# Kernel optimization log

Hardware: AMD Instinct MI355X
Metric: run time of the kernel (lower is better)

The kernel has to match this reference:

```python
import jax, jax.numpy as jnp
from jax import lax
import numpy as np

DIM = 256
D_STATE = 16
D_CONV = 4
EXPAND = 2
D_INNER = EXPAND * DIM          # 512
DT_RANK = (DIM + 15) // 16      # 16
EPS = 1e-5


def setup_inputs() -> dict:
    key = jax.random.key(0)
    ks = jax.random.split(key, 8)
    B, H, W = 8, 32, 32
    dt_init = 0.01  # softplus(b_dt) ~= dt_init at init (mamba-style)
    return {
        "x": jax.random.normal(ks[0], (B, DIM, H, W), jnp.float32),
        "ln_gamma": jnp.ones((DIM,), jnp.float32),
        "ln_beta": jnp.zeros((DIM,), jnp.float32),
        "W_in": jax.random.normal(ks[1], (DIM, 2 * D_INNER), jnp.float32) * 0.02,
        "conv_w": jax.random.normal(ks[2], (D_INNER, D_CONV), jnp.float32) * 0.2,
        "conv_b": jnp.zeros((D_INNER,), jnp.float32),
        "W_xproj": jax.random.normal(ks[3], (D_INNER, DT_RANK + 2 * D_STATE), jnp.float32) * 0.02,
        "W_dt": jax.random.normal(ks[4], (DT_RANK, D_INNER), jnp.float32) * 0.05,
        "b_dt": jnp.full((D_INNER,), float(np.log(np.expm1(dt_init))), jnp.float32),
        "A_log": jnp.log(jnp.broadcast_to(
            jnp.arange(1, D_STATE + 1, dtype=jnp.float32), (D_INNER, D_STATE))),
        "D_skip": jnp.ones((D_INNER,), jnp.float32),
        "W_out": jax.random.normal(ks[5], (D_INNER, DIM), jnp.float32) * 0.02,
    }


def _mamba_layer(x, ln_gamma, ln_beta, W_in, conv_w, conv_b, W_xproj,
                 W_dt, b_dt, A_log, D_skip, W_out):
    B, C, H, W = x.shape
    L = H * W
    # (B,C,H,W) -> (B, L, C)
    xf = x.transpose(0, 2, 3, 1).reshape(B, L, C)
    # LayerNorm over channel dim
    mu = xf.mean(-1, keepdims=True)
    var = ((xf - mu) ** 2).mean(-1, keepdims=True)
    xn = (xf - mu) * lax.rsqrt(var + EPS) * ln_gamma + ln_beta
    # in_proj -> u (ssm branch) and z (gate branch)
    xz = xn @ W_in                              # [B, L, 2*D_INNER]
    u, z = xz[..., :D_INNER], xz[..., D_INNER:]
    # causal depthwise conv1d over L, then SiLU
    uc = u.transpose(0, 2, 1)                   # [B, D_INNER, L]
    uc = lax.conv_general_dilated(
        uc, conv_w[:, None, :], window_strides=(1,),
        padding=[(D_CONV - 1, 0)], feature_group_count=D_INNER)
    u2 = jax.nn.silu(uc + conv_b[None, :, None]).transpose(0, 2, 1)  # [B, L, D_INNER]
    # input-dependent dt, B, C
    dbc = u2 @ W_xproj                          # [B, L, DT_RANK + 2*D_STATE]
    dt = jax.nn.softplus(dbc[..., :DT_RANK] @ W_dt + b_dt)            # [B, L, D_INNER]
    Bm = dbc[..., DT_RANK:DT_RANK + D_STATE]    # [B, L, D_STATE]
    Cm = dbc[..., DT_RANK + D_STATE:]           # [B, L, D_STATE]
    A = -jnp.exp(A_log)                         # [D_INNER, D_STATE]

    def step(h, ins):
        dt_t, B_t, C_t, u_t = ins               # [B,Din], [B,S], [B,S], [B,Din]
        dA = jnp.exp(dt_t[:, :, None] * A)      # [B, Din, S]
        h = dA * h + dt_t[:, :, None] * B_t[:, None, :] * u_t[:, :, None]
        y = jnp.einsum('bds,bs->bd', h, C_t)
        return h, y

    h0 = jnp.zeros((B, D_INNER, D_STATE), xf.dtype)
    xs = (dt.transpose(1, 0, 2), Bm.transpose(1, 0, 2),
          Cm.transpose(1, 0, 2), u2.transpose(1, 0, 2))
    _, ys = lax.scan(step, h0, xs)              # ys: [L, B, D_INNER]
    y = ys.transpose(1, 0, 2) + u2 * D_skip     # skip connection D*u
    y = y * jax.nn.silu(z)                      # gate
    o = y @ W_out                               # [B, L, C]
    return o.reshape(B, H, W, C).transpose(0, 3, 1, 2) + x


def reference(x, ln_gamma, ln_beta, W_in, conv_w, conv_b, W_xproj,
              W_dt, b_dt, A_log, D_skip, W_out):
    return _mamba_layer(x, ln_gamma, ln_beta, W_in, conv_w, conv_b, W_xproj,
                        W_dt, b_dt, A_log, D_skip, W_out)
```

## Files before the change

### kernel.cpp

```cpp
#include <hip/hip_runtime.h>
#include <hip/hip_bf16.h>
#include <math.h>

#define DIMC   256
#define DI     512
#define DS     16
#define DTR    16
#define NX     48
#define BATCH  8
#define LSEQ   1024
#define MROWS  8192
#define CHUNK  64
#define NC     (LSEQ / CHUNK)

typedef __attribute__((ext_vector_type(8))) short short8;
typedef __attribute__((ext_vector_type(4))) float f32x4;

__device__ __forceinline__ unsigned short f2bf(float v) {
  __hip_bfloat16 h = __float2bfloat16(v);
  return *reinterpret_cast<unsigned short*>(&h);
}

__device__ __forceinline__ float dpp_sum16(float v) {
  float t;
  t = __int_as_float(__builtin_amdgcn_mov_dpp(__float_as_int(v), 0xB1,  0xF, 0xF, true)); v += t;
  t = __int_as_float(__builtin_amdgcn_mov_dpp(__float_as_int(v), 0x4E,  0xF, 0xF, true)); v += t;
  t = __int_as_float(__builtin_amdgcn_mov_dpp(__float_as_int(v), 0x141, 0xF, 0xF, true)); v += t;
  t = __int_as_float(__builtin_amdgcn_mov_dpp(__float_as_int(v), 0x140, 0xF, 0xF, true)); v += t;
  return v;
}

__global__ __launch_bounds__(256) void prep_all(const float* __restrict__ W_in,
                                                const float* __restrict__ W_out,
                                                const float* __restrict__ W_xproj,
                                                const float* __restrict__ W_dt,
                                                unsigned short* __restrict__ Wib,
                                                unsigned short* __restrict__ Wob,
                                                unsigned short* __restrict__ Wxpb,
                                                unsigned short* __restrict__ Wdtb) {
  __shared__ float t[32][33];
  const int blk = blockIdx.x, tid = threadIdx.x;
  if (blk < 384) {
    const float* W; unsigned short* Wt; int K, N, bx, by;
    if (blk < 256) { W = W_in;  Wt = Wib; K = DIMC; N = 1024; bx = blk & 31; by = blk >> 5; }
    else           { W = W_out; Wt = Wob; K = DI;   N = DIMC; bx = (blk - 256) & 7; by = (blk - 256) >> 3; }
    int n0 = bx * 32, k0 = by * 32;
    int tx = tid & 31, ty = tid >> 5;
    for (int i = ty; i < 32; i += 8) t[i][tx] = W[(size_t)(k0 + i) * N + n0 + tx];
    __syncthreads();
    for (int i = ty; i < 32; i += 8)
      Wt[(size_t)(n0 + i) * K + k0 + tx] = f2bf(t[tx][i]);
  } else if (blk < 512) {
    int idx = (blk - 384) * 256 + tid;
    int n = idx >> 9, k = idx & 511;
    Wxpb[idx] = (n < NX) ? f2bf(W_xproj[(size_t)k * NX + n]) : (unsigned short)0;
  } else {
    int idx = (blk - 512) * 256 + tid;
    int n = idx >> 5, k = idx & 31;
    Wdtb[idx] = (k < DTR) ? f2bf(W_dt[(size_t)k * DI + n]) : (unsigned short)0;
  }
}

__global__ __launch_bounds__(256) void ln_kernel(const float* __restrict__ x,
                                                 const float* __restrict__ gamma,
                                                 const float* __restrict__ beta,
                                                 unsigned short* __restrict__ xnb) {
  __shared__ float sx[DIMC][67];
  __shared__ float smean[64], srs[64];
  const int b = blockIdx.y, l0 = blockIdx.x * 64;
  const int tid = threadIdx.x;
  {
    const int cbase = tid >> 2;
    const int lp = (tid & 3) * 16;
#pragma unroll
    for (int cg = 0; cg < 4; ++cg) {
      const int c = cg * 64 + cbase;
      const float* p = x + ((size_t)b * DIMC + c) * LSEQ + l0 + lp;
#pragma unroll
      for (int q = 0; q < 4; ++q) {
        float4 v = *(const float4*)(p + q * 4);
        sx[c][lp + q * 4 + 0] = v.x;
        sx[c][lp + q * 4 + 1] = v.y;
        sx[c][lp + q * 4 + 2] = v.z;
        sx[c][lp + q * 4 + 3] = v.w;
      }
    }
  }
  __syncthreads();
  {
    const int lane = tid & 63, w = tid >> 6;
    const int l = (w << 4) + (lane & 15);
    const int quad = lane >> 4;
    float sum = 0.f, sq = 0.f;
#pragma unroll 8
    for (int cc = 0; cc < 64; ++cc) {
      float v = sx[quad * 64 + cc][l];
      sum += v; sq += v * v;
    }
    sum += __shfl_xor(sum, 16); sq += __shfl_xor(sq, 16);
    sum += __shfl_xor(sum, 32); sq += __shfl_xor(sq, 32);
    if (quad == 0) {
      float mean = sum * (1.f / 256.f);
      float var  = sq * (1.f / 256.f) - mean * mean;
      smean[l] = mean; srs[l] = rsqrtf(var + 1e-5f);
    }
  }
  __syncthreads();
  {
    const float gg = gamma[tid], bb = beta[tid];
    const size_t base = ((size_t)b * LSEQ + l0) * DIMC + tid;
#pragma unroll 4
    for (int ll = 0; ll < 64; ++ll) {
      float v = (sx[tid][ll] - smean[ll]) * srs[ll] * gg + bb;
      xnb[base + (size_t)ll * DIMC] = f2bf(v);
    }
  }
}

#define GTM 128
#define GTN 64
#define GBK 32
__global__ __launch_bounds__(256) void gemm_bf16(const unsigned short* __restrict__ A,
                                                 const unsigned short* __restrict__ Bt,
                                                 float* __restrict__ C,
                                                 int M, int N, int K, int mode,
                                                 const float* __restrict__ X) {
  __shared__ unsigned short As[GTM][GBK];
  __shared__ unsigned short Bs[GTN][GBK];
  const int tid = threadIdx.x;
  const int lane = tid & 63, wave = tid >> 6;
  const int wm = wave >> 1, wn = wave & 1;
  const int quad = lane >> 4, l16 = lane & 15;
  const int m0 = blockIdx.y * GTM, n0 = blockIdx.x * GTN;

  f32x4 acc[4][2];
#pragma unroll
  for (int i = 0; i < 4; ++i)
#pragma unroll
    for (int j = 0; j < 2; ++j) acc[i][j] = (f32x4){0.f, 0.f, 0.f, 0.f};

  for (int k0 = 0; k0 < K; k0 += GBK) {
#pragma unroll
    for (int q = 0; q < 2; ++q) {
      int id = q * 256 + tid;
      int row = id >> 2, c = id & 3;
      uint4 v = *(const uint4*)(A + (size_t)(m0 + row) * K + k0 + c * 8);
      *(uint4*)&As[row][c * 8] = v;
    }
    {
      int row = tid >> 2, c = tid & 3;
      uint4 v = *(const uint4*)(Bt + (size_t)(n0 + row) * K + k0 + c * 8);
      *(uint4*)&Bs[row][c * 8] = v;
    }
    __syncthreads();
    short8 af[4], bfrag[2];
#pragma unroll
    for (int i = 0; i < 4; ++i)
      af[i] = *(const short8*)&As[wm * 64 + i * 16 + l16][quad * 8];
#pragma unroll
    for (int j = 0; j < 2; ++j)
      bfrag[j] = *(const short8*)&Bs[wn * 32 + j * 16 + l16][quad * 8];
#pragma unroll
    for (int i = 0; i < 4; ++i)
#pragma unroll
      for (int j = 0; j < 2; ++j)
        acc[i][j] = __builtin_amdgcn_mfma_f32_16x16x32_bf16(af[i], bfrag[j], acc[i][j], 0, 0, 0);
    __syncthreads();
  }

  if (mode == 0) {
#pragma unroll
    for (int i = 0; i < 4; ++i) {
      int rowb = wm * 64 + i * 16 + quad * 4;
#pragma unroll
      for (int j = 0; j < 2; ++j) {
        int n = n0 + wn * 32 + j * 16 + l16;
#pragma unroll
        for (int r = 0; r < 4; ++r)
          C[(size_t)(m0 + rowb + r) * N + n] = acc[i][j][r];
      }
    }
  } else {
#pragma unroll
    for (int i = 0; i < 4; ++i) {
      int m = m0 + wm * 64 + i * 16 + quad * 4;
      int b = m >> 10, l = m & 1023;
#pragma unroll
      for (int j = 0; j < 2; ++j) {
        int n = n0 + wn * 32 + j * 16 + l16;
        size_t o = (size_t)b * (DIMC * LSEQ) + (size_t)n * LSEQ + l;
        f32x4 xv = *(const f32x4*)(X + o);
        f32x4 rv = acc[i][j] + xv;
        *(f32x4*)(C + o) = rv;
      }
    }
  }
}

__global__ __launch_bounds__(256) void conv_silu(const float* __restrict__ xz,
                                                 const float* __restrict__ conv_w,
                                                 const float* __restrict__ conv_b,
                                                 float* __restrict__ u2,
                                                 unsigned int* __restrict__ u2b) {
  int idx = (blockIdx.x * 256 + threadIdx.x) * 2;
  int c = idx & (DI - 1);
  int m = idx >> 9;
  int l = m & 1023;
  float2 acc = *(const float2*)(conv_b + c);
  float4 w0 = *(const float4*)(conv_w + c * 4);
  float4 w1 = *(const float4*)(conv_w + c * 4 + 4);
  const float wa[4] = {w0.x, w0.y, w0.z, w0.w};
  const float wb[4] = {w1.x, w1.y, w1.z, w1.w};
#pragma unroll
  for (int k = 0; k < 4; ++k) {
    int lj = l - 3 + k;
    if (lj >= 0) {
      float2 v = *(const float2*)(xz + (size_t)(m - 3 + k) * 1024 + c);
      acc.x = fmaf(v.x, wa[k], acc.x);
      acc.y = fmaf(v.y, wb[k], acc.y);
    }
  }
  float vx = acc.x / (1.f + __expf(-acc.x));
  float vy = acc.y / (1.f + __expf(-acc.y));
  *(float2*)(u2 + idx) = make_float2(vx, vy);
  u2b[idx >> 1] = (unsigned int)f2bf(vx) | ((unsigned int)f2bf(vy) << 16);
}

__global__ __launch_bounds__(256) void xproj_dt(const unsigned short* __restrict__ u2b,
                                                const unsigned short* __restrict__ Wxpb,
                                                const unsigned short* __restrict__ Wdtb,
                                                const float* __restrict__ b_dt,
                                                float* __restrict__ dbc64,
                                                float* __restrict__ dtv) {
  __shared__ unsigned short Bs[64][512 + 8];
  __shared__ unsigned short sdbc[32][40];
  const int m0 = blockIdx.x * 32;
  const int tid = threadIdx.x, lane = tid & 63, w = tid >> 6;
  const int quad = lane >> 4, l16 = lane & 15;
#pragma unroll
  for (int q = 0; q < 16; ++q) {
    int id = q * 256 + tid;
    int row = id >> 6, c8 = id & 63;
    *(uint4*)&Bs[row][c8 * 8] = *(const uint4*)(Wxpb + (size_t)row * 512 + c8 * 8);
  }
  __syncthreads();
  f32x4 acc[2];
  acc[0] = (f32x4){0.f, 0.f, 0.f, 0.f};
  acc[1] = (f32x4){0.f, 0.f, 0.f, 0.f};
#pragma unroll 4
  for (int k0 = 0; k0 < 512; k0 += 32) {
    short8 af0 = *(const short8*)(u2b + (size_t)(m0 + l16) * 512 + k0 + quad * 8);
    short8 af1 = *(const short8*)(u2b + (size_t)(m0 + 16 + l16) * 512 + k0 + quad * 8);
    short8 bf  = *(const short8*)&Bs[w * 16 + l16][k0 + quad * 8];
    acc[0] = __builtin_amdgcn_mfma_f32_16x16x32_bf16(af0, bf, acc[0], 0, 0, 0);
    acc[1] = __builtin_amdgcn_mfma_f32_16x16x32_bf16(af1, bf, acc[1], 0, 0, 0);
  }
#pragma unroll
  for (int i = 0; i < 2; ++i)
#pragma unroll
    for (int r = 0; r < 4; ++r)
      dbc64[(size_t)(m0 + i * 16 + quad * 4 + r) * 64 + w * 16 + l16] = acc[i][r];
  if (w < 2) {
#pragma unroll
    for (int i = 0; i < 2; ++i)
#pragma unroll
      for (int r = 0; r < 4; ++r)
        sdbc[i * 16 + quad * 4 + r][w * 16 + l16] = f2bf(acc[i][r]);
  }
  __syncthreads();
  short8 af0 = *(const short8*)&sdbc[l16][quad * 8];
  short8 af1 = *(const short8*)&sdbc[16 + l16][quad * 8];
#pragma unroll
  for (int jn = 0; jn < 8; ++jn) {
    const int n0 = w * 128 + jn * 16;
    short8 bf = *(const short8*)(Wdtb + (size_t)(n0 + l16) * 32 + quad * 8);
    f32x4 a0 = (f32x4){0.f, 0.f, 0.f, 0.f}, a1 = a0;
    a0 = __builtin_amdgcn_mfma_f32_16x16x32_bf16(af0, bf, a0, 0, 0, 0);
    a1 = __builtin_amdgcn_mfma_f32_16x16x32_bf16(af1, bf, a1, 0, 0, 0);
    const float bd = b_dt[n0 + l16];
#pragma unroll
    for (int r = 0; r < 4; ++r) {
      float v = a0[r] + bd;
      dtv[(size_t)(m0 + quad * 4 + r) * DI + n0 + l16] = (v > 20.f) ? v : log1pf(__expf(v));
      float v2 = a1[r] + bd;
      dtv[(size_t)(m0 + 16 + quad * 4 + r) * DI + n0 + l16] = (v2 > 20.f) ? v2 : log1pf(__expf(v2));
    }
  }
}

__global__ __launch_bounds__(256) void scan_pass1(const float* __restrict__ dtv,
                                                  const float* __restrict__ u2,
                                                  const float* __restrict__ dbc64,
                                                  const float* __restrict__ A_log,
                                                  float* __restrict__ hend,
                                                  float* __restrict__ Ssum) {
  const int bb = blockIdx.x, dblk = blockIdx.y, cc = blockIdx.z;
  const int tid = threadIdx.x;
  const int di = tid >> 4, s = tid & 15;
  const int d = dblk * 16 + di;
  const float Ads = -__expf(A_log[d * DS + s]);

  __shared__ float2 sdu[CHUNK][16];
  __shared__ float  sB[CHUNK][16];
  {
    const int t0 = cc * CHUNK;
#pragma unroll
    for (int q = 0; q < 4; ++q) {
      int lin = q * 256 + tid;
      int tt = lin >> 4, dd = lin & 15;
      size_t m = (size_t)bb * LSEQ + t0 + tt;
      sdu[tt][dd] = make_float2(dtv[m * DI + dblk * 16 + dd], u2[m * DI + dblk * 16 + dd]);
      sB[tt][dd]  = dbc64[m * 64 + DTR + dd];
    }
  }
  __syncthreads();
  float h = 0.f, dtsum = 0.f;
#pragma unroll 4
  for (int tt = 0; tt < CHUNK; ++tt) {
    float2 du = sdu[tt][di];
    float Bv  = sB[tt][s];
    h = fmaf(__expf(du.x * Ads), h, du.x * du.y * Bv);
    dtsum += du.x;
  }
  size_t ci = ((size_t)(bb * NC + cc) * DI + d);
  hend[ci * DS + s] = h;
  if (s == 0) Ssum[ci] = dtsum;
}

__global__ __launch_bounds__(256) void scan_pass2(const float* __restrict__ A_log,
                                                  const float* __restrict__ hend,
                                                  const float* __restrict__ Ssum,
                                                  float* __restrict__ hin) {
  const int bb = blockIdx.x, dblk = blockIdx.y;
  const int tid = threadIdx.x;
  const int di = tid >> 4, s = tid & 15;
  const int d = dblk * 16 + di;
  const float Ads = -__expf(A_log[d * DS + s]);
  float h = 0.f;
  for (int cc = 0; cc < NC; ++cc) {
    size_t ci = ((size_t)(bb * NC + cc) * DI + d);
    hin[ci * DS + s] = h;
    h = fmaf(__expf(Ads * Ssum[ci]), h, hend[ci * DS + s]);
  }
}

__global__ __launch_bounds__(256) void scan_pass3(const float* __restrict__ dtv,
                                                  const float* __restrict__ u2,
                                                  const float* __restrict__ dbc64,
                                                  const float* __restrict__ xz,
                                                  const float* __restrict__ A_log,
                                                  const float* __restrict__ D_skip,
                                                  const float* __restrict__ hin,
                                                  unsigned short* __restrict__ yb) {
  const int bb = blockIdx.x, dblk = blockIdx.y, cc = blockIdx.z;
  const int tid = threadIdx.x;
  const int di = tid >> 4, s = tid & 15;
  const int d = dblk * 16 + di;
  const float Ads = -__expf(A_log[d * DS + s]);

  __shared__ float2 sdu[CHUNK][16];
  __shared__ float2 sBC[CHUNK][16];
  __shared__ float  sz[CHUNK][16], sy[CHUNK][16];
  const int t0 = cc * CHUNK;
#pragma unroll
  for (int q = 0; q < 4; ++q) {
    int lin = q * 256 + tid;
    int tt = lin >> 4, dd = lin & 15;
    size_t m = (size_t)bb * LSEQ + t0 + tt;
    sdu[tt][dd] = make_float2(dtv[m * DI + dblk * 16 + dd], u2[m * DI + dblk * 16 + dd]);
    sBC[tt][dd] = make_float2(dbc64[m * 64 + DTR + dd], dbc64[m * 64 + DTR + DS + dd]);
    sz [tt][dd] = xz[m * 1024 + DI + dblk * 16 + dd];
  }
  __syncthreads();
  float h = hin[((size_t)(bb * NC + cc) * DI + d) * DS + s];
#pragma unroll 4
  for (int tt = 0; tt < CHUNK; ++tt) {
    float2 du = sdu[tt][di];
    float2 bc = sBC[tt][s];
    h = fmaf(__expf(du.x * Ads), h, du.x * du.y * bc.x);
    float v = dpp_sum16(h * bc.y);
    if (s == 0) sy[tt][di] = v;
  }
  __syncthreads();
#pragma unroll
  for (int q = 0; q < 4; ++q) {
    int lin = q * 256 + tid;
    int tt = lin >> 4, dd = lin & 15;
    size_t m = (size_t)bb * LSEQ + t0 + tt;
    float yv = sy[tt][dd] + sdu[tt][dd].y * D_skip[dblk * 16 + dd];
    float z = sz[tt][dd];
    yv *= z / (1.f + __expf(-z));
    yb[m * DI + dblk * 16 + dd] = f2bf(yv);
  }
}

extern "C" void kernel_launch(void* const* d_in, const int* in_sizes, int n_in,
                              void* d_out, int out_size, void* d_ws, size_t ws_size,
                              hipStream_t stream) {
  const float* x       = (const float*)d_in[0];
  const float* ln_g    = (const float*)d_in[1];
  const float* ln_b    = (const float*)d_in[2];
  const float* W_in    = (const float*)d_in[3];
  const float* conv_w  = (const float*)d_in[4];
  const float* conv_b  = (const float*)d_in[5];
  const float* W_xproj = (const float*)d_in[6];
  const float* W_dt    = (const float*)d_in[7];
  const float* b_dt    = (const float*)d_in[8];
  const float* A_log   = (const float*)d_in[9];
  const float* D_skip  = (const float*)d_in[10];
  const float* W_out   = (const float*)d_in[11];
  float* out = (float*)d_out;

  float* ws    = (float*)d_ws;
  float* xz    = ws;
  float* u2    = xz   + (size_t)MROWS * 1024;
  float* dbc64 = u2   + (size_t)MROWS * DI;
  float* dtv   = dbc64 + (size_t)MROWS * 64;
  float* hend  = dtv  + (size_t)MROWS * DI;
  float* hin   = hend + (size_t)BATCH * NC * DI * DS;
  float* Ssum  = hin  + (size_t)BATCH * NC * DI * DS;
  unsigned short* u2b  = (unsigned short*)(Ssum + (size_t)BATCH * NC * DI);
  unsigned short* yb   = u2b + (size_t)MROWS * DI;
  unsigned short* xnb  = yb;
  unsigned short* Wib  = yb  + (size_t)MROWS * DI;
  unsigned short* Wob  = Wib + (size_t)DIMC * 1024;
  unsigned short* Wxpb = Wob + (size_t)DI * DIMC;
  unsigned short* Wdtb = Wxpb + (size_t)64 * 512;

  prep_all<<<576, 256, 0, stream>>>(W_in, W_out, W_xproj, W_dt, Wib, Wob, Wxpb, Wdtb);

  ln_kernel<<<dim3(LSEQ / 64, BATCH), 256, 0, stream>>>(x, ln_g, ln_b, xnb);

  gemm_bf16<<<dim3(1024 / GTN, MROWS / GTM), 256, 0, stream>>>(
      xnb, Wib, xz, MROWS, 1024, DIMC, 0, nullptr);

  conv_silu<<<(MROWS * DI) / 512, 256, 0, stream>>>(xz, conv_w, conv_b, u2,
                                                    (unsigned int*)u2b);

  xproj_dt<<<MROWS / 32, 256, 0, stream>>>(u2b, Wxpb, Wdtb, b_dt, dbc64, dtv);

  dim3 gp13(BATCH, DI / 16, NC);
  dim3 gp2(BATCH, DI / 16);
  scan_pass1<<<gp13, 256, 0, stream>>>(dtv, u2, dbc64, A_log, hend, Ssum);
  scan_pass2<<<gp2, 256, 0, stream>>>(A_log, hend, Ssum, hin);
  scan_pass3<<<gp13, 256, 0, stream>>>(dtv, u2, dbc64, xz, A_log, D_skip, hin, yb);

  gemm_bf16<<<dim3(DIMC / GTN, MROWS / GTM), 256, 0, stream>>>(
      yb, Wob, out, MROWS, DIMC, DI, 1, x);
}
```

Baseline: 212.2 us.

## Give each scan thread four states and 64 channels per block

Scan passes 1 and 3 now map each thread to one channel and four of the sixteen states, so a block covers 64 channels instead of 16. The shared-memory staging of dt, u, B, C and z is dropped in favour of direct global loads, with float4 reads for B and C. The output reduction across states shrinks from a 16-lane to a 4-lane DPP sum, and the gating epilogue reads z and u straight from global memory. The grid for these passes shrinks by four, which lowers parallelism and adds per-step global loads in the serial loop, in exchange for less redundant per-thread work and fewer cross-lane operations.

```diff
diff --git a/kernel.cpp b/kernel.cpp
--- a/kernel.cpp
+++ b/kernel.cpp
@@ -21,12 +21,10 @@
   return *reinterpret_cast<unsigned short*>(&h);
 }
 
-__device__ __forceinline__ float dpp_sum16(float v) {
+__device__ __forceinline__ float dpp_sum4(float v) {
   float t;
-  t = __int_as_float(__builtin_amdgcn_mov_dpp(__float_as_int(v), 0xB1,  0xF, 0xF, true)); v += t;
-  t = __int_as_float(__builtin_amdgcn_mov_dpp(__float_as_int(v), 0x4E,  0xF, 0xF, true)); v += t;
-  t = __int_as_float(__builtin_amdgcn_mov_dpp(__float_as_int(v), 0x141, 0xF, 0xF, true)); v += t;
-  t = __int_as_float(__builtin_amdgcn_mov_dpp(__float_as_int(v), 0x140, 0xF, 0xF, true)); v += t;
+  t = __int_as_float(__builtin_amdgcn_mov_dpp(__float_as_int(v), 0xB1, 0xF, 0xF, true)); v += t;
+  t = __int_as_float(__builtin_amdgcn_mov_dpp(__float_as_int(v), 0x4E, 0xF, 0xF, true)); v += t;
   return v;
 }
 
@@ -296,35 +294,29 @@
                                                   float* __restrict__ Ssum) {
   const int bb = blockIdx.x, dblk = blockIdx.y, cc = blockIdx.z;
   const int tid = threadIdx.x;
-  const int di = tid >> 4, s = tid & 15;
-  const int d = dblk * 16 + di;
-  const float Ads = -__expf(A_log[d * DS + s]);
-
-  __shared__ float2 sdu[CHUNK][16];
-  __shared__ float  sB[CHUNK][16];
-  {
-    const int t0 = cc * CHUNK;
-#pragma unroll
-    for (int q = 0; q < 4; ++q) {
-      int lin = q * 256 + tid;
-      int tt = lin >> 4, dd = lin & 15;
-      size_t m = (size_t)bb * LSEQ + t0 + tt;
-      sdu[tt][dd] = make_float2(dtv[m * DI + dblk * 16 + dd], u2[m * DI + dblk * 16 + dd]);
-      sB[tt][dd]  = dbc64[m * 64 + DTR + dd];
-    }
-  }
-  __syncthreads();
-  float h = 0.f, dtsum = 0.f;
+  const int dl = tid >> 2, q = tid & 3;
+  const int d = dblk * 64 + dl;
+  float4 Av = *(const float4*)(A_log + d * DS + q * 4);
+  float Ads[4] = {-__expf(Av.x), -__expf(Av.y), -__expf(Av.z), -__expf(Av.w)};
+  float h[4] = {0.f, 0.f, 0.f, 0.f};
+  float dtsum = 0.f;
+  const size_t mbase = (size_t)bb * LSEQ + cc * CHUNK;
 #pragma unroll 4
   for (int tt = 0; tt < CHUNK; ++tt) {
-    float2 du = sdu[tt][di];
-    float Bv  = sB[tt][s];
-    h = fmaf(__expf(du.x * Ads), h, du.x * du.y * Bv);
-    dtsum += du.x;
+    size_t m = mbase + tt;
+    float dtt = dtv[m * DI + d];
+    float uu  = u2 [m * DI + d];
+    float4 Bv = *(const float4*)(dbc64 + m * 64 + DTR + q * 4);
+    float common = dtt * uu;
+    h[0] = fmaf(__expf(dtt * Ads[0]), h[0], common * Bv.x);
+    h[1] = fmaf(__expf(dtt * Ads[1]), h[1], common * Bv.y);
+    h[2] = fmaf(__expf(dtt * Ads[2]), h[2], common * Bv.z);
+    h[3] = fmaf(__expf(dtt * Ads[3]), h[3], common * Bv.w);
+    dtsum += dtt;
   }
   size_t ci = ((size_t)(bb * NC + cc) * DI + d);
-  hend[ci * DS + s] = h;
-  if (s == 0) Ssum[ci] = dtsum;
+  *(float4*)(hend + ci * DS + q * 4) = make_float4(h[0], h[1], h[2], h[3]);
+  if (q == 0) Ssum[ci] = dtsum;
 }
 
 __global__ __launch_bounds__(256) void scan_pass2(const float* __restrict__ A_log,
@@ -352,45 +344,46 @@
                                                   const float* __restrict__ D_skip,
                                                   const float* __restrict__ hin,
                                                   unsigned short* __restrict__ yb) {
+  __shared__ float sy[CHUNK][64];
   const int bb = blockIdx.x, dblk = blockIdx.y, cc = blockIdx.z;
   const int tid = threadIdx.x;
-  const int di = tid >> 4, s = tid & 15;
-  const int d = dblk * 16 + di;
-  const float Ads = -__expf(A_log[d * DS + s]);
-
-  __shared__ float2 sdu[CHUNK][16];
-  __shared__ float2 sBC[CHUNK][16];
-  __shared__ float  sz[CHUNK][16], sy[CHUNK][16];
-  const int t0 = cc * CHUNK;
-#pragma unroll
-  for (int q = 0; q < 4; ++q) {
-    int lin = q * 256 + tid;
-    int tt = lin >> 4, dd = lin & 15;
-    size_t m = (size_t)bb * LSEQ + t0 + tt;
-    sdu[tt][dd] = make_float2(dtv[m * DI + dblk * 16 + dd], u2[m * DI + dblk * 16 + dd]);
-    sBC[tt][dd] = make_float2(dbc64[m * 64 + DTR + dd], dbc64[m * 64 + DTR + DS + dd]);
-    sz [tt][dd] = xz[m * 1024 + DI + dblk * 16 + dd];
-  }
-  __syncthreads();
-  float h = hin[((size_t)(bb * NC + cc) * DI + d) * DS + s];
+  const int dl = tid >> 2, q = tid & 3;
+  const int d = dblk * 64 + dl;
+  float4 Av = *(const float4*)(A_log + d * DS + q * 4);
+  float Ads[4] = {-__expf(Av.x), -__expf(Av.y), -__expf(Av.z), -__expf(Av.w)};
+  const size_t ci = ((size_t)(bb * NC + cc) * DI + d);
+  float4 h4 = *(const float4*)(hin + ci * DS + q * 4);
+  float h[4] = {h4.x, h4.y, h4.z, h4.w};
+  const size_t mbase = (size_t)bb * LSEQ + cc * CHUNK;
 #pragma unroll 4
   for (int tt = 0; tt < CHUNK; ++tt) {
-    float2 du = sdu[tt][di];
-    float2 bc = sBC[tt][s];
-    h = fmaf(__expf(du.x * Ads), h, du.x * du.y * bc.x);
-    float v = dpp_sum16(h * bc.y);
-    if (s == 0) sy[tt][di] = v;
+    size_t m = mbase + tt;
+    float dtt = dtv[m * DI + d];
+    float uu  = u2 [m * DI + d];
+    float4 Bv = *(const float4*)(dbc64 + m * 64 + DTR + q * 4);
+    float4 Cv = *(const float4*)(dbc64 + m * 64 + DTR + DS + q * 4);
+    float common = dtt * uu;
+    float yp;
+    h[0] = fmaf(__expf(dtt * Ads[0]), h[0], common * Bv.x); yp  = h[0] * Cv.x;
+    h[1] = fmaf(__expf(dtt * Ads[1]), h[1], common * Bv.y); yp = fmaf(h[1], Cv.y, yp);
+    h[2] = fmaf(__expf(dtt * Ads[2]), h[2], common * Bv.z); yp = fmaf(h[2], Cv.z, yp);
+    h[3] = fmaf(__expf(dtt * Ads[3]), h[3], common * Bv.w); yp = fmaf(h[3], Cv.w, yp);
+    yp = dpp_sum4(yp);
+    if (q == 0) sy[tt][dl] = yp;
   }
   __syncthreads();
-#pragma unroll
-  for (int q = 0; q < 4; ++q) {
-    int lin = q * 256 + tid;
-    int tt = lin >> 4, dd = lin & 15;
-    size_t m = (size_t)bb * LSEQ + t0 + tt;
-    float yv = sy[tt][dd] + sdu[tt][dd].y * D_skip[dblk * 16 + dd];
-    float z = sz[tt][dd];
+  const int ed = tid & 63, tq = tid >> 6;
+  const int dg = dblk * 64 + ed;
+  const float dsk = D_skip[dg];
+#pragma unroll 4
+  for (int it = 0; it < 16; ++it) {
+    int tt = it * 4 + tq;
+    size_t m = mbase + tt;
+    float z  = xz[m * 1024 + DI + dg];
+    float uu = u2[m * DI + dg];
+    float yv = sy[tt][ed] + uu * dsk;
     yv *= z / (1.f + __expf(-z));
-    yb[m * DI + dblk * 16 + dd] = f2bf(yv);
+    yb[m * DI + dg] = f2bf(yv);
   }
 }
 
@@ -439,7 +432,7 @@
 
   xproj_dt<<<MROWS / 32, 256, 0, stream>>>(u2b, Wxpb, Wdtb, b_dt, dbc64, dtv);
 
-  dim3 gp13(BATCH, DI / 16, NC);
+  dim3 gp13(BATCH, DI / 64, NC);
   dim3 gp2(BATCH, DI / 16);
   scan_pass1<<<gp13, 256, 0, stream>>>(dtv, u2, dbc64, A_log, hend, Ssum);
   scan_pass2<<<gp2, 256, 0, stream>>>(A_log, hend, Ssum, hin);
```

Result: slower. 220.2 us (+3.8%).

## Merge weight prep with LayerNorm and fold inter-chunk scan into pass3

Applied to the files above, without the earlier changes.

Weight conversion and LayerNorm now run in one prologue kernel using extra block indices. The separate scan_pass2 kernel is removed. Each pass3 block recomputes its incoming chunk state by looping over all earlier chunk summaries, overlapped with its shared-memory loads. This cuts two kernel launches and the hin buffer round trip, at the cost of redundant serial work that grows with chunk index, up to 15 steps.

```diff
diff --git a/kernel.cpp b/kernel.cpp
--- a/kernel.cpp
+++ b/kernel.cpp
@@ -30,17 +30,23 @@
   return v;
 }
 
-__global__ __launch_bounds__(256) void prep_all(const float* __restrict__ W_in,
+__global__ __launch_bounds__(256) void prologue(const float* __restrict__ W_in,
                                                 const float* __restrict__ W_out,
                                                 const float* __restrict__ W_xproj,
                                                 const float* __restrict__ W_dt,
+                                                const float* __restrict__ x,
+                                                const float* __restrict__ gamma,
+                                                const float* __restrict__ beta,
                                                 unsigned short* __restrict__ Wib,
                                                 unsigned short* __restrict__ Wob,
                                                 unsigned short* __restrict__ Wxpb,
-                                                unsigned short* __restrict__ Wdtb) {
-  __shared__ float t[32][33];
+                                                unsigned short* __restrict__ Wdtb,
+                                                unsigned short* __restrict__ xnb) {
+  __shared__ float sx[DIMC][67];
+  __shared__ float smean[64], srs[64];
   const int blk = blockIdx.x, tid = threadIdx.x;
   if (blk < 384) {
+    float (*t)[67] = sx;
     const float* W; unsigned short* Wt; int K, N, bx, by;
     if (blk < 256) { W = W_in;  Wt = Wib; K = DIMC; N = 1024; bx = blk & 31; by = blk >> 5; }
     else           { W = W_out; Wt = Wob; K = DI;   N = DIMC; bx = (blk - 256) & 7; by = (blk - 256) >> 3; }
@@ -50,25 +56,22 @@
     __syncthreads();
     for (int i = ty; i < 32; i += 8)
       Wt[(size_t)(n0 + i) * K + k0 + tx] = f2bf(t[tx][i]);
-  } else if (blk < 512) {
+    return;
+  }
+  if (blk < 512) {
     int idx = (blk - 384) * 256 + tid;
     int n = idx >> 9, k = idx & 511;
     Wxpb[idx] = (n < NX) ? f2bf(W_xproj[(size_t)k * NX + n]) : (unsigned short)0;
-  } else {
+    return;
+  }
+  if (blk < 576) {
     int idx = (blk - 512) * 256 + tid;
     int n = idx >> 5, k = idx & 31;
     Wdtb[idx] = (k < DTR) ? f2bf(W_dt[(size_t)k * DI + n]) : (unsigned short)0;
-  }
-}
-
-__global__ __launch_bounds__(256) void ln_kernel(const float* __restrict__ x,
-                                                 const float* __restrict__ gamma,
-                                                 const float* __restrict__ beta,
-                                                 unsigned short* __restrict__ xnb) {
-  __shared__ float sx[DIMC][67];
-  __shared__ float smean[64], srs[64];
-  const int b = blockIdx.y, l0 = blockIdx.x * 64;
-  const int tid = threadIdx.x;
+    return;
+  }
+  const int lb = blk - 576;
+  const int b = lb >> 4, l0 = (lb & 15) * 64;
   {
     const int cbase = tid >> 2;
     const int lp = (tid & 3) * 16;
@@ -327,30 +330,14 @@
   if (s == 0) Ssum[ci] = dtsum;
 }
 
-__global__ __launch_bounds__(256) void scan_pass2(const float* __restrict__ A_log,
-                                                  const float* __restrict__ hend,
-                                                  const float* __restrict__ Ssum,
-                                                  float* __restrict__ hin) {
-  const int bb = blockIdx.x, dblk = blockIdx.y;
-  const int tid = threadIdx.x;
-  const int di = tid >> 4, s = tid & 15;
-  const int d = dblk * 16 + di;
-  const float Ads = -__expf(A_log[d * DS + s]);
-  float h = 0.f;
-  for (int cc = 0; cc < NC; ++cc) {
-    size_t ci = ((size_t)(bb * NC + cc) * DI + d);
-    hin[ci * DS + s] = h;
-    h = fmaf(__expf(Ads * Ssum[ci]), h, hend[ci * DS + s]);
-  }
-}
-
 __global__ __launch_bounds__(256) void scan_pass3(const float* __restrict__ dtv,
                                                   const float* __restrict__ u2,
                                                   const float* __restrict__ dbc64,
                                                   const float* __restrict__ xz,
                                                   const float* __restrict__ A_log,
                                                   const float* __restrict__ D_skip,
-                                                  const float* __restrict__ hin,
+                                                  const float* __restrict__ hend,
+                                                  const float* __restrict__ Ssum,
                                                   unsigned short* __restrict__ yb) {
   const int bb = blockIdx.x, dblk = blockIdx.y, cc = blockIdx.z;
   const int tid = threadIdx.x;
@@ -371,8 +358,12 @@
     sBC[tt][dd] = make_float2(dbc64[m * 64 + DTR + dd], dbc64[m * 64 + DTR + DS + dd]);
     sz [tt][dd] = xz[m * 1024 + DI + dblk * 16 + dd];
   }
-  __syncthreads();
-  float h = hin[((size_t)(bb * NC + cc) * DI + d) * DS + s];
+  float h = 0.f;
+  for (int j = 0; j < cc; ++j) {
+    size_t cj = ((size_t)(bb * NC + j) * DI + d);
+    h = fmaf(__expf(Ads * Ssum[cj]), h, hend[cj * DS + s]);
+  }
+  __syncthreads();
 #pragma unroll 4
   for (int tt = 0; tt < CHUNK; ++tt) {
     float2 du = sdu[tt][di];
@@ -417,8 +408,7 @@
   float* dbc64 = u2   + (size_t)MROWS * DI;
   float* dtv   = dbc64 + (size_t)MROWS * 64;
   float* hend  = dtv  + (size_t)MROWS * DI;
-  float* hin   = hend + (size_t)BATCH * NC * DI * DS;
-  float* Ssum  = hin  + (size_t)BATCH * NC * DI * DS;
+  float* Ssum  = hend + (size_t)BATCH * NC * DI * DS;
   unsigned short* u2b  = (unsigned short*)(Ssum + (size_t)BATCH * NC * DI);
   unsigned short* yb   = u2b + (size_t)MROWS * DI;
   unsigned short* xnb  = yb;
@@ -427,9 +417,8 @@
   unsigned short* Wxpb = Wob + (size_t)DI * DIMC;
   unsigned short* Wdtb = Wxpb + (size_t)64 * 512;
 
-  prep_all<<<576, 256, 0, stream>>>(W_in, W_out, W_xproj, W_dt, Wib, Wob, Wxpb, Wdtb);
-
-  ln_kernel<<<dim3(LSEQ / 64, BATCH), 256, 0, stream>>>(x, ln_g, ln_b, xnb);
+  prologue<<<704, 256, 0, stream>>>(W_in, W_out, W_xproj, W_dt, x, ln_g, ln_b,
+                                    Wib, Wob, Wxpb, Wdtb, xnb);
 
   gemm_bf16<<<dim3(1024 / GTN, MROWS / GTM), 256, 0, stream>>>(
       xnb, Wib, xz, MROWS, 1024, DIMC, 0, nullptr);
@@ -440,10 +429,9 @@
   xproj_dt<<<MROWS / 32, 256, 0, stream>>>(u2b, Wxpb, Wdtb, b_dt, dbc64, dtv);
 
   dim3 gp13(BATCH, DI / 16, NC);
-  dim3 gp2(BATCH, DI / 16);
   scan_pass1<<<gp13, 256, 0, stream>>>(dtv, u2, dbc64, A_log, hend, Ssum);
-  scan_pass2<<<gp2, 256, 0, stream>>>(A_log, hend, Ssum, hin);
-  scan_pass3<<<gp13, 256, 0, stream>>>(dtv, u2, dbc64, xz, A_log, D_skip, hin, yb);
+  scan_pass3<<<gp13, 256, 0, stream>>>(dtv, u2, dbc64, xz, A_log, D_skip,
+                                       hend, Ssum, yb);
 
   gemm_bf16<<<dim3(DIMC / GTN, MROWS / GTM), 256, 0, stream>>>(
       yb, Wob, out, MROWS, DIMC, DI, 1, x);
```

Result: slower. 216.7 us (+2.1%).
